# Performance work log

Measured on AMD Instinct MI355X. Metric: run time of the kernel, lower is better.

## Reference

```python
import jax, jax.numpy as jnp
import numpy as np

N_NODES = 100000
N_EDGES = 3200000
F_IN = 128
F_OUT = 128


def setup_inputs() -> dict:
    key = jax.random.key(0)
    k1, k2, k3 = jax.random.split(key, 3)
    x = jax.random.normal(k1, (N_NODES, F_IN), dtype=jnp.float32)
    edge_index = jax.random.randint(k2, (2, N_EDGES), 0, N_NODES, dtype=jnp.int64)
    # xavier_uniform for weight, zeros for bias
    limit = float(np.sqrt(6.0 / (F_IN + F_OUT)))
    weight = jax.random.uniform(k3, (F_IN, F_OUT), dtype=jnp.float32,
                                minval=-limit, maxval=limit)
    bias = jnp.zeros((F_OUT,), dtype=jnp.float32)
    return {"x": x, "edge_index": edge_index, "weight": weight, "bias": bias}


def reference(x, edge_index, weight, bias):
    num_nodes = x.shape[0]
    # add self loops
    loops = jnp.arange(num_nodes, dtype=edge_index.dtype)
    row = jnp.concatenate([edge_index[0], loops])  # [E+N]
    col = jnp.concatenate([edge_index[1], loops])  # [E+N]
    # degree from row (matches torch.bincount(row))
    deg = jnp.zeros((num_nodes,), dtype=x.dtype).at[row].add(1.0)
    deg_inv_sqrt = jnp.where(deg > 0, jax.lax.rsqrt(jnp.maximum(deg, 1.0)), 0.0)
    norm = deg_inv_sqrt[row] * deg_inv_sqrt[col]  # [E+N]
    # dense transform then sparse aggregation (gather-scale-scatter)
    support = x @ weight  # [N, F_OUT]
    msgs = support[col] * norm[:, None]  # [E+N, F_OUT]
    out = jax.ops.segment_sum(msgs, row, num_segments=num_nodes)
    return out + bias
```

## Files before the change

kernel.cpp:

```cpp
#include <hip/hip_runtime.h>
#include <hip/hip_fp16.h>

#define FDIM 128
#define SCAN_B 1024
#define NBUK 8
#define NCHK 32
#define MAXB 12544
#define NFB (NBUK * NCHK)

typedef _Float16 half8 __attribute__((ext_vector_type(8)));
typedef float f32x4 __attribute__((ext_vector_type(4)));

__global__ void __launch_bounds__(1024) k_cnt(const int* __restrict__ row,
                                              int* __restrict__ cntC,
                                              int nE, int n, int bspan) {
    __shared__ int hist[MAXB];
    int bucket = blockIdx.x & (NBUK - 1);
    int chunk  = blockIdx.x >> 3;
    int lo  = bucket * bspan;
    int len = min(bspan, n - lo);
    for (int j = threadIdx.x; j < len; j += 1024) hist[j] = 0;
    __syncthreads();

    int per = (((nE + NCHK - 1) / NCHK) + 3) & ~3;
    int beg = chunk * per;
    int end = min(beg + per, nE);
    if (beg < end) {
        int nv = (end - beg) >> 2;
        const int4* row4 = reinterpret_cast<const int4*>(row + beg);
        for (int q = threadIdx.x; q < nv; q += 1024) {
            int4 r = row4[q];
            unsigned a;
            a = (unsigned)(r.x - lo); if (a < (unsigned)len) atomicAdd(&hist[a], 1);
            a = (unsigned)(r.y - lo); if (a < (unsigned)len) atomicAdd(&hist[a], 1);
            a = (unsigned)(r.z - lo); if (a < (unsigned)len) atomicAdd(&hist[a], 1);
            a = (unsigned)(r.w - lo); if (a < (unsigned)len) atomicAdd(&hist[a], 1);
        }
        for (int e = beg + (nv << 2) + threadIdx.x; e < end; e += 1024) {
            unsigned a = (unsigned)(row[e] - lo);
            if (a < (unsigned)len) atomicAdd(&hist[a], 1);
        }
    }
    __syncthreads();
    int* dst = cntC + (size_t)chunk * n + lo;
    for (int j = threadIdx.x; j < len; j += 1024) dst[j] = hist[j];
}

__global__ void __launch_bounds__(1024) k_scan_reduce(const int* __restrict__ cntC,
                                                      int* __restrict__ part, int n) {
    __shared__ int sd[1024];
    int i = blockIdx.x * SCAN_B + threadIdx.x;
    int v = 0;
    if (i < n) {
        v = 1;
        #pragma unroll
        for (int c = 0; c < NCHK; ++c) v += cntC[(size_t)c * n + i];
    }
    sd[threadIdx.x] = v;
    __syncthreads();
    for (int off = 512; off > 0; off >>= 1) {
        if (threadIdx.x < off) sd[threadIdx.x] += sd[threadIdx.x + off];
        __syncthreads();
    }
    if (threadIdx.x == 0) part[blockIdx.x] = sd[0];
}

__global__ void __launch_bounds__(1024) k_scan_final(int* __restrict__ cntC,
                                                     const int* __restrict__ part,
                                                     int* __restrict__ offs,
                                                     float* __restrict__ dis,
                                                     int* __restrict__ sc,
                                                     int n, int nb) {
    __shared__ int sd[1024];
    __shared__ int sdp[128];
    int pv = 0;
    if (threadIdx.x < 128) {
        pv = (threadIdx.x < nb) ? part[threadIdx.x] : 0;
        sdp[threadIdx.x] = pv;
    }
    __syncthreads();
    for (int off = 1; off < 128; off <<= 1) {
        int t = 0;
        if (threadIdx.x < 128 && threadIdx.x >= off) t = sdp[threadIdx.x - off];
        __syncthreads();
        if (threadIdx.x < 128) sdp[threadIdx.x] += t;
        __syncthreads();
    }
    int blockbase = (blockIdx.x == 0) ? 0 : sdp[blockIdx.x - 1];

    int i = blockIdx.x * SCAN_B + threadIdx.x;
    int c[NCHK];
    int v = 0;
    if (i < n) {
        v = 1;
        #pragma unroll
        for (int x = 0; x < NCHK; ++x) { c[x] = cntC[(size_t)x * n + i]; v += c[x]; }
    }
    sd[threadIdx.x] = v;
    __syncthreads();
    for (int off = 1; off < 1024; off <<= 1) {
        int t = (threadIdx.x >= off) ? sd[threadIdx.x - off] : 0;
        __syncthreads();
        sd[threadIdx.x] += t;
        __syncthreads();
    }
    if (i < n) {
        int o = blockbase + sd[threadIdx.x] - v;
        offs[i] = o;
        if (i == n - 1) offs[n] = o + v;
        dis[i]  = rsqrtf((float)v);
        sc[o]   = i;
        int b = o + 1;
        #pragma unroll
        for (int x = 0; x < NCHK; ++x) { cntC[(size_t)x * n + i] = b; b += c[x]; }
    }
}

__global__ void __launch_bounds__(1024) k_fuse(const int* __restrict__ row,
                                               const int* __restrict__ col,
                                               int* __restrict__ curC,
                                               int* __restrict__ sc,
                                               const float* __restrict__ x,
                                               const float* __restrict__ w,
                                               const float* __restrict__ dis,
                                               __half* __restrict__ support,
                                               int nE, int n, int bspan) {
    __shared__ char smraw[65536];

    if (blockIdx.x < NFB) {
        int* cur = reinterpret_cast<int*>(smraw);
        int bucket = blockIdx.x & (NBUK - 1);
        int chunk  = blockIdx.x >> 3;
        int lo  = bucket * bspan;
        int len = min(bspan, n - lo);
        const int* src = curC + (size_t)chunk * n + lo;
        for (int j = threadIdx.x; j < len; j += 1024) cur[j] = src[j];
        __syncthreads();

        int per = (((nE + NCHK - 1) / NCHK) + 3) & ~3;
        int beg = chunk * per;
        int end = min(beg + per, nE);
        if (beg < end) {
            int nv = (end - beg) >> 2;
            const int4* row4 = reinterpret_cast<const int4*>(row + beg);
            const int4* col4 = reinterpret_cast<const int4*>(col + beg);
            for (int q = threadIdx.x; q < nv; q += 1024) {
                int4 r  = row4[q];
                int4 cc = col4[q];
                unsigned a;
                a = (unsigned)(r.x - lo); if (a < (unsigned)len) sc[atomicAdd(&cur[a], 1)] = cc.x;
                a = (unsigned)(r.y - lo); if (a < (unsigned)len) sc[atomicAdd(&cur[a], 1)] = cc.y;
                a = (unsigned)(r.z - lo); if (a < (unsigned)len) sc[atomicAdd(&cur[a], 1)] = cc.z;
                a = (unsigned)(r.w - lo); if (a < (unsigned)len) sc[atomicAdd(&cur[a], 1)] = cc.w;
            }
            for (int e = beg + (nv << 2) + threadIdx.x; e < end; e += 1024) {
                unsigned a = (unsigned)(row[e] - lo);
                if (a < (unsigned)len) sc[atomicAdd(&cur[a], 1)] = col[e];
            }
        }
    } else {
        half8* smw = reinterpret_cast<half8*>(smraw);
        for (int e = threadIdx.x; e < 2048; e += 1024) {
            int fid = e >> 6, lane = e & 63;
            int nt = fid >> 2, ks = fid & 3;
            int f  = nt * 16 + (lane & 15);
            int k0 = ks * 32 + (lane >> 4) * 8;
            half8 hi, lo;
            #pragma unroll
            for (int j = 0; j < 8; ++j) {
                float v = w[(size_t)(k0 + j) * FDIM + f];
                _Float16 h = (_Float16)v;
                hi[j] = h;
                lo[j] = (_Float16)(v - (float)h);
            }
            smw[e]        = hi;
            smw[2048 + e] = lo;
        }
        __syncthreads();

        int wave = threadIdx.x >> 6;
        int lane = threadIdx.x & 63;
        int wbase = (blockIdx.x - NFB) * 256 + wave * 16;
        if (wbase >= n) return;
        int r  = lane & 15;
        int kg = lane >> 4;

        int noder = min(wbase + r, n - 1);
        const float* xp = x + (size_t)noder * FDIM + kg * 8;
        half8 ah[4], al[4];
        #pragma unroll
        for (int ks = 0; ks < 4; ++ks) {
            const float4* p = reinterpret_cast<const float4*>(xp + ks * 32);
            float4 f0 = p[0], f1 = p[1];
            float v[8] = {f0.x, f0.y, f0.z, f0.w, f1.x, f1.y, f1.z, f1.w};
            #pragma unroll
            for (int j = 0; j < 8; ++j) {
                _Float16 h = (_Float16)v[j];
                ah[ks][j] = h;
                al[ks][j] = (_Float16)(v[j] - (float)h);
            }
        }

        float d[4];
        #pragma unroll
        for (int i = 0; i < 4; ++i)
            d[i] = dis[min(wbase + kg * 4 + i, n - 1)];

        #pragma unroll
        for (int nt = 0; nt < 8; ++nt) {
            const half8* bp = smw + (size_t)(nt * 4) * 64 + lane;
            f32x4 acc = {0.f, 0.f, 0.f, 0.f};
            #pragma unroll
            for (int ks = 0; ks < 4; ++ks) {
                half8 bh = bp[ks * 64];
                half8 bl = bp[2048 + ks * 64];
                acc = __builtin_amdgcn_mfma_f32_16x16x32_f16(ah[ks], bh, acc, 0, 0, 0);
                acc = __builtin_amdgcn_mfma_f32_16x16x32_f16(al[ks], bh, acc, 0, 0, 0);
                acc = __builtin_amdgcn_mfma_f32_16x16x32_f16(ah[ks], bl, acc, 0, 0, 0);
            }
            #pragma unroll
            for (int i = 0; i < 4; ++i) {
                int node = wbase + kg * 4 + i;
                if (node < n)
                    support[(size_t)node * FDIM + nt * 16 + r] =
                        __float2half(d[i] * acc[i]);
            }
        }
    }
}

__global__ void __launch_bounds__(64) k_agg(const __half2* __restrict__ sup2,
                                            const int* __restrict__ offs,
                                            const int* __restrict__ sc,
                                            const float* __restrict__ dis,
                                            const float* __restrict__ bias,
                                            float* __restrict__ out, int n) {
    int i  = blockIdx.x;
    int f2 = threadIdx.x;
    int beg = offs[i], end = offs[i + 1];
    float ax = 0.f, ay = 0.f;
    int j = beg;
    for (; j + 8 <= end; j += 8) {
        int c0 = sc[j],     c1 = sc[j + 1], c2 = sc[j + 2], c3 = sc[j + 3];
        int c4 = sc[j + 4], c5 = sc[j + 5], c6 = sc[j + 6], c7 = sc[j + 7];
        float2 v0 = __half22float2(sup2[(size_t)c0 * 64 + f2]);
        float2 v1 = __half22float2(sup2[(size_t)c1 * 64 + f2]);
        float2 v2 = __half22float2(sup2[(size_t)c2 * 64 + f2]);
        float2 v3 = __half22float2(sup2[(size_t)c3 * 64 + f2]);
        float2 v4 = __half22float2(sup2[(size_t)c4 * 64 + f2]);
        float2 v5 = __half22float2(sup2[(size_t)c5 * 64 + f2]);
        float2 v6 = __half22float2(sup2[(size_t)c6 * 64 + f2]);
        float2 v7 = __half22float2(sup2[(size_t)c7 * 64 + f2]);
        ax += ((v0.x + v1.x) + (v2.x + v3.x)) + ((v4.x + v5.x) + (v6.x + v7.x));
        ay += ((v0.y + v1.y) + (v2.y + v3.y)) + ((v4.y + v5.y) + (v6.y + v7.y));
    }
    for (; j + 4 <= end; j += 4) {
        int c0 = sc[j], c1 = sc[j + 1], c2 = sc[j + 2], c3 = sc[j + 3];
        float2 v0 = __half22float2(sup2[(size_t)c0 * 64 + f2]);
        float2 v1 = __half22float2(sup2[(size_t)c1 * 64 + f2]);
        float2 v2 = __half22float2(sup2[(size_t)c2 * 64 + f2]);
        float2 v3 = __half22float2(sup2[(size_t)c3 * 64 + f2]);
        ax += (v0.x + v1.x) + (v2.x + v3.x);
        ay += (v0.y + v1.y) + (v2.y + v3.y);
    }
    for (; j < end; ++j) {
        float2 v = __half22float2(sup2[(size_t)sc[j] * 64 + f2]);
        ax += v.x; ay += v.y;
    }
    float di = dis[i];
    const float2* b2 = reinterpret_cast<const float2*>(bias);
    float2 bb = b2[f2];
    float2 o;
    o.x = di * ax + bb.x;
    o.y = di * ay + bb.y;
    reinterpret_cast<float2*>(out)[(size_t)i * 64 + f2] = o;
}

extern "C" void kernel_launch(void* const* d_in, const int* in_sizes, int n_in,
                              void* d_out, int out_size, void* d_ws, size_t ws_size,
                              hipStream_t stream) {
    const float* x    = (const float*)d_in[0];
    const int*   ei   = (const int*)d_in[1];
    const float* w    = (const float*)d_in[2];
    const float* bias = (const float*)d_in[3];
    float*       out  = (float*)d_out;

    int n  = in_sizes[0] / FDIM;
    int nE = in_sizes[1] / 2;
    const int* row = ei;
    const int* col = ei + nE;
    int nbscan = (n + SCAN_B - 1) / SCAN_B;
    int bspan  = (n + NBUK - 1) / NBUK;
    int ngb    = (n + 255) / 256;

    char* ws = (char*)d_ws;
    size_t off = 0;
    auto alloc = [&](size_t bytes) -> void* {
        void* p = ws + off;
        off += (bytes + 255) & ~(size_t)255;
        return p;
    };
    __half* support = (__half*)alloc((size_t)n * FDIM * sizeof(__half));
    int*    cntC    = (int*)alloc((size_t)NCHK * n * sizeof(int));
    int*    offs    = (int*)alloc((size_t)(n + 1) * sizeof(int));
    int*    part    = (int*)alloc((size_t)128 * sizeof(int));
    float*  dis     = (float*)alloc((size_t)n * sizeof(float));
    int*    sc      = (int*)alloc((size_t)(nE + n) * sizeof(int));

    k_cnt        <<<NBUK * NCHK, 1024, 0, stream>>>(row, cntC, nE, n, bspan);
    k_scan_reduce<<<nbscan, 1024, 0, stream>>>(cntC, part, n);
    k_scan_final <<<nbscan, 1024, 0, stream>>>(cntC, part, offs, dis, sc, n, nbscan);
    k_fuse       <<<NFB + ngb, 1024, 0, stream>>>(row, col, cntC, sc,
                                                  x, w, dis, support, nE, n, bspan);
    k_agg        <<<n, 64, 0, stream>>>((const __half2*)support, offs,
                                        sc, dis, bias, out, n);
}
```

Before: 322.2 us.

## Pack per-chunk node counters into bytes and cut edge re-reads to two halves

```diff
diff --git a/kernel.cpp b/kernel.cpp
--- a/kernel.cpp
+++ b/kernel.cpp
@@ -3,23 +3,23 @@
 
 #define FDIM 128
 #define SCAN_B 1024
-#define NBUK 8
-#define NCHK 32
-#define MAXB 12544
-#define NFB (NBUK * NCHK)
+#define NCHK 128
+#define NHALF 2
+#define NFB (NHALF * NCHK)
 
 typedef _Float16 half8 __attribute__((ext_vector_type(8)));
 typedef float f32x4 __attribute__((ext_vector_type(4)));
 
 __global__ void __launch_bounds__(1024) k_cnt(const int* __restrict__ row,
-                                              int* __restrict__ cntC,
-                                              int nE, int n, int bspan) {
-    __shared__ int hist[MAXB];
-    int bucket = blockIdx.x & (NBUK - 1);
-    int chunk  = blockIdx.x >> 3;
-    int lo  = bucket * bspan;
-    int len = min(bspan, n - lo);
-    for (int j = threadIdx.x; j < len; j += 1024) hist[j] = 0;
+                                              unsigned char* __restrict__ cnt8,
+                                              int nE, int n, int hspan) {
+    __shared__ unsigned int h32[12544];
+    int half  = blockIdx.x & (NHALF - 1);
+    int chunk = blockIdx.x >> 1;
+    int lo  = half * hspan;
+    int len = min(hspan, n - lo);
+    int nw  = (len + 3) >> 2;
+    for (int j = threadIdx.x; j < nw; j += 1024) h32[j] = 0;
     __syncthreads();
 
     int per = (((nE + NCHK - 1) / NCHK) + 3) & ~3;
@@ -31,30 +31,31 @@
         for (int q = threadIdx.x; q < nv; q += 1024) {
             int4 r = row4[q];
             unsigned a;
-            a = (unsigned)(r.x - lo); if (a < (unsigned)len) atomicAdd(&hist[a], 1);
-            a = (unsigned)(r.y - lo); if (a < (unsigned)len) atomicAdd(&hist[a], 1);
-            a = (unsigned)(r.z - lo); if (a < (unsigned)len) atomicAdd(&hist[a], 1);
-            a = (unsigned)(r.w - lo); if (a < (unsigned)len) atomicAdd(&hist[a], 1);
+            a = (unsigned)(r.x - lo); if (a < (unsigned)len) atomicAdd(&h32[a >> 2], 1u << ((a & 3) << 3));
+            a = (unsigned)(r.y - lo); if (a < (unsigned)len) atomicAdd(&h32[a >> 2], 1u << ((a & 3) << 3));
+            a = (unsigned)(r.z - lo); if (a < (unsigned)len) atomicAdd(&h32[a >> 2], 1u << ((a & 3) << 3));
+            a = (unsigned)(r.w - lo); if (a < (unsigned)len) atomicAdd(&h32[a >> 2], 1u << ((a & 3) << 3));
         }
         for (int e = beg + (nv << 2) + threadIdx.x; e < end; e += 1024) {
             unsigned a = (unsigned)(row[e] - lo);
-            if (a < (unsigned)len) atomicAdd(&hist[a], 1);
-        }
-    }
-    __syncthreads();
-    int* dst = cntC + (size_t)chunk * n + lo;
-    for (int j = threadIdx.x; j < len; j += 1024) dst[j] = hist[j];
-}
-
-__global__ void __launch_bounds__(1024) k_scan_reduce(const int* __restrict__ cntC,
+            if (a < (unsigned)len) atomicAdd(&h32[a >> 2], 1u << ((a & 3) << 3));
+        }
+    }
+    __syncthreads();
+    unsigned int* dst = reinterpret_cast<unsigned int*>(cnt8 + (size_t)chunk * n + lo);
+    for (int j = threadIdx.x; j < nw; j += 1024) dst[j] = h32[j];
+}
+
+__global__ void __launch_bounds__(1024) k_scan_reduce(const unsigned char* __restrict__ cnt8,
                                                       int* __restrict__ part, int n) {
     __shared__ int sd[1024];
     int i = blockIdx.x * SCAN_B + threadIdx.x;
     int v = 0;
     if (i < n) {
         v = 1;
-        #pragma unroll
-        for (int c = 0; c < NCHK; ++c) v += cntC[(size_t)c * n + i];
+        const unsigned char* p = cnt8 + i;
+        #pragma unroll 16
+        for (int c = 0; c < NCHK; ++c) v += p[(size_t)c * n];
     }
     sd[threadIdx.x] = v;
     __syncthreads();
@@ -65,7 +66,7 @@
     if (threadIdx.x == 0) part[blockIdx.x] = sd[0];
 }
 
-__global__ void __launch_bounds__(1024) k_scan_final(int* __restrict__ cntC,
+__global__ void __launch_bounds__(1024) k_scan_final(unsigned char* __restrict__ cnt8,
                                                      const int* __restrict__ part,
                                                      int* __restrict__ offs,
                                                      float* __restrict__ dis,
@@ -89,12 +90,12 @@
     int blockbase = (blockIdx.x == 0) ? 0 : sdp[blockIdx.x - 1];
 
     int i = blockIdx.x * SCAN_B + threadIdx.x;
-    int c[NCHK];
     int v = 0;
     if (i < n) {
         v = 1;
-        #pragma unroll
-        for (int x = 0; x < NCHK; ++x) { c[x] = cntC[(size_t)x * n + i]; v += c[x]; }
+        const unsigned char* p = cnt8 + i;
+        #pragma unroll 16
+        for (int c = 0; c < NCHK; ++c) v += p[(size_t)c * n];
     }
     sd[threadIdx.x] = v;
     __syncthreads();
@@ -110,31 +111,39 @@
         if (i == n - 1) offs[n] = o + v;
         dis[i]  = rsqrtf((float)v);
         sc[o]   = i;
-        int b = o + 1;
-        #pragma unroll
-        for (int x = 0; x < NCHK; ++x) { cntC[(size_t)x * n + i] = b; b += c[x]; }
+        unsigned char* p = cnt8 + i;
+        int b = 1;
+        #pragma unroll 16
+        for (int c = 0; c < NCHK; ++c) {
+            unsigned char cb = p[(size_t)c * n];
+            p[(size_t)c * n] = (unsigned char)b;
+            b += cb;
+        }
     }
 }
 
 __global__ void __launch_bounds__(1024) k_fuse(const int* __restrict__ row,
                                                const int* __restrict__ col,
-                                               int* __restrict__ curC,
+                                               unsigned char* __restrict__ cnt8,
+                                               const int* __restrict__ offs,
                                                int* __restrict__ sc,
                                                const float* __restrict__ x,
                                                const float* __restrict__ w,
                                                const float* __restrict__ dis,
                                                __half* __restrict__ support,
-                                               int nE, int n, int bspan) {
+                                               int nE, int n, int hspan) {
     __shared__ char smraw[65536];
 
     if (blockIdx.x < NFB) {
-        int* cur = reinterpret_cast<int*>(smraw);
-        int bucket = blockIdx.x & (NBUK - 1);
-        int chunk  = blockIdx.x >> 3;
-        int lo  = bucket * bspan;
-        int len = min(bspan, n - lo);
-        const int* src = curC + (size_t)chunk * n + lo;
-        for (int j = threadIdx.x; j < len; j += 1024) cur[j] = src[j];
+        unsigned int* cur32 = reinterpret_cast<unsigned int*>(smraw);
+        int half  = blockIdx.x & (NHALF - 1);
+        int chunk = blockIdx.x >> 1;
+        int lo  = half * hspan;
+        int len = min(hspan, n - lo);
+        int nw  = (len + 3) >> 2;
+        const unsigned int* src = reinterpret_cast<const unsigned int*>(
+            cnt8 + (size_t)chunk * n + lo);
+        for (int j = threadIdx.x; j < nw; j += 1024) cur32[j] = src[j];
         __syncthreads();
 
         int per = (((nE + NCHK - 1) / NCHK) + 3) & ~3;
@@ -147,15 +156,40 @@
             for (int q = threadIdx.x; q < nv; q += 1024) {
                 int4 r  = row4[q];
                 int4 cc = col4[q];
-                unsigned a;
-                a = (unsigned)(r.x - lo); if (a < (unsigned)len) sc[atomicAdd(&cur[a], 1)] = cc.x;
-                a = (unsigned)(r.y - lo); if (a < (unsigned)len) sc[atomicAdd(&cur[a], 1)] = cc.y;
-                a = (unsigned)(r.z - lo); if (a < (unsigned)len) sc[atomicAdd(&cur[a], 1)] = cc.z;
-                a = (unsigned)(r.w - lo); if (a < (unsigned)len) sc[atomicAdd(&cur[a], 1)] = cc.w;
+                unsigned a, old, sh;
+                a = (unsigned)(r.x - lo);
+                if (a < (unsigned)len) {
+                    sh = (a & 3) << 3;
+                    old = atomicAdd(&cur32[a >> 2], 1u << sh);
+                    sc[offs[r.x] + (int)((old >> sh) & 255u)] = cc.x;
+                }
+                a = (unsigned)(r.y - lo);
+                if (a < (unsigned)len) {
+                    sh = (a & 3) << 3;
+                    old = atomicAdd(&cur32[a >> 2], 1u << sh);
+                    sc[offs[r.y] + (int)((old >> sh) & 255u)] = cc.y;
+                }
+                a = (unsigned)(r.z - lo);
+                if (a < (unsigned)len) {
+                    sh = (a & 3) << 3;
+                    old = atomicAdd(&cur32[a >> 2], 1u << sh);
+                    sc[offs[r.z] + (int)((old >> sh) & 255u)] = cc.z;
+                }
+                a = (unsigned)(r.w - lo);
+                if (a < (unsigned)len) {
+                    sh = (a & 3) << 3;
+                    old = atomicAdd(&cur32[a >> 2], 1u << sh);
+                    sc[offs[r.w] + (int)((old >> sh) & 255u)] = cc.w;
+                }
             }
             for (int e = beg + (nv << 2) + threadIdx.x; e < end; e += 1024) {
-                unsigned a = (unsigned)(row[e] - lo);
-                if (a < (unsigned)len) sc[atomicAdd(&cur[a], 1)] = col[e];
+                int r = row[e];
+                unsigned a = (unsigned)(r - lo);
+                if (a < (unsigned)len) {
+                    unsigned sh = (a & 3) << 3;
+                    unsigned old = atomicAdd(&cur32[a >> 2], 1u << sh);
+                    sc[offs[r] + (int)((old >> sh) & 255u)] = col[e];
+                }
             }
         }
     } else {
@@ -290,7 +324,7 @@
     const int* row = ei;
     const int* col = ei + nE;
     int nbscan = (n + SCAN_B - 1) / SCAN_B;
-    int bspan  = (n + NBUK - 1) / NBUK;
+    int hspan  = (((n + NHALF - 1) / NHALF) + 3) & ~3;
     int ngb    = (n + 255) / 256;
 
     char* ws = (char*)d_ws;
@@ -300,18 +334,18 @@
         off += (bytes + 255) & ~(size_t)255;
         return p;
     };
-    __half* support = (__half*)alloc((size_t)n * FDIM * sizeof(__half));
-    int*    cntC    = (int*)alloc((size_t)NCHK * n * sizeof(int));
-    int*    offs    = (int*)alloc((size_t)(n + 1) * sizeof(int));
-    int*    part    = (int*)alloc((size_t)128 * sizeof(int));
-    float*  dis     = (float*)alloc((size_t)n * sizeof(float));
-    int*    sc      = (int*)alloc((size_t)(nE + n) * sizeof(int));
-
-    k_cnt        <<<NBUK * NCHK, 1024, 0, stream>>>(row, cntC, nE, n, bspan);
-    k_scan_reduce<<<nbscan, 1024, 0, stream>>>(cntC, part, n);
-    k_scan_final <<<nbscan, 1024, 0, stream>>>(cntC, part, offs, dis, sc, n, nbscan);
-    k_fuse       <<<NFB + ngb, 1024, 0, stream>>>(row, col, cntC, sc,
-                                                  x, w, dis, support, nE, n, bspan);
+    __half*        support = (__half*)alloc((size_t)n * FDIM * sizeof(__half));
+    unsigned char* cnt8    = (unsigned char*)alloc((size_t)NCHK * n + 16);
+    int*           offs    = (int*)alloc((size_t)(n + 1) * sizeof(int));
+    int*           part    = (int*)alloc((size_t)128 * sizeof(int));
+    float*         dis     = (float*)alloc((size_t)n * sizeof(float));
+    int*           sc      = (int*)alloc((size_t)(nE + n) * sizeof(int));
+
+    k_cnt        <<<NFB, 1024, 0, stream>>>(row, cnt8, nE, n, hspan);
+    k_scan_reduce<<<nbscan, 1024, 0, stream>>>(cnt8, part, n);
+    k_scan_final <<<nbscan, 1024, 0, stream>>>(cnt8, part, offs, dis, sc, n, nbscan);
+    k_fuse       <<<NFB + ngb, 1024, 0, stream>>>(row, col, cnt8, offs, sc,
+                                                  x, w, dis, support, nE, n, hspan);
     k_agg        <<<n, 64, 0, stream>>>((const __half2*)support, offs,
                                         sc, dis, bias, out, n);
 }
```

Result: no change. 322.2 us (-0.0%).
